# Kernel tuning notes

Measured on AMD Instinct MI355X. Metric: run time of the kernel, lower is better.

## Reference

```python
import jax, jax.numpy as jnp
import numpy as np

MARGIN = 0.3


def _l2norm(x, axis=-1):
    return x / (jnp.linalg.norm(x, axis=axis, keepdims=True) + 1e-12)


def setup_inputs() -> dict:
    key = jax.random.key(0)
    k1, k2, k3, k4 = jax.random.split(key, 4)
    n, P, d = 1024, 8, 2048
    global_feat = jax.random.normal(k1, (n, d), dtype=jnp.float32)
    partial_feat = jax.random.normal(k2, (n, P, d), dtype=jnp.float32)
    part_labels = jax.random.randint(k3, (n, P), 0, 2).astype(jnp.float32)
    global_labels = jax.random.randint(k4, (n,), 0, 64).astype(jnp.int64)
    return {"global_feat": global_feat, "partial_feat": partial_feat,
            "part_labels": part_labels, "global_labels": global_labels}


def reference(global_feat, partial_feat, part_labels, global_labels):
    # --- compute_distance (VGTripletLoss) ---
    g = _l2norm(global_feat)            # [n, d]
    p = _l2norm(partial_feat)           # [n, P, d]
    gs = (1.0 - g @ g.T) / 2.0          # [n, n]
    overlap = part_labels[:, None, :] * part_labels[None, :, :]   # [n, n, P]
    # per-part cosine distance: [n, n, P]
    slf = (1.0 - jnp.einsum('ipd,jpd->ijp', p, p)) / 2.0
    slf = slf * overlap
    dist = (slf.sum(-1) + gs) / (overlap.sum(-1) + 1.0)            # [n, n]

    # --- compute_loss: hard positive/negative mining ---
    mask = global_labels[:, None] == global_labels[None, :]        # [n, n]
    neg_inf = jnp.float32(-1e30)
    pos_inf = jnp.float32(1e30)
    dist_ap = jnp.max(jnp.where(mask, dist, neg_inf), axis=1)      # hardest positive
    dist_an = jnp.min(jnp.where(mask, pos_inf, dist), axis=1)      # hardest negative
    # MarginRankingLoss(y=1, reduction='mean'): max(0, dist_ap - dist_an + margin)
    loss = jnp.mean(jax.nn.relu(dist_ap - dist_an + MARGIN))
    return loss
```

## Files before the change

kernel.cpp:

```cpp
#include <hip/hip_runtime.h>

#define N 1024
#define D 2048
#define P 8
#define F 9
#define KTOT (F * D)
#define BM 128
#define BKT 32
#define MARGIN 0.3f

typedef float f32x4 __attribute__((ext_vector_type(4)));
typedef short s16x8 __attribute__((ext_vector_type(8)));

#define GLOBAL_AS __attribute__((address_space(1)))
#define LDS_AS __attribute__((address_space(3)))

__device__ __forceinline__ const float* feat_row(const float* __restrict__ g,
                                                 const float* __restrict__ p,
                                                 int i, int f) {
    return (f == 0) ? (g + (size_t)i * D)
                    : (p + ((size_t)i * P + (f - 1)) * D);
}

__device__ __forceinline__ unsigned f2bf(float x) {
    unsigned u = __float_as_uint(x);
    return (u + 0x7fffu + ((u >> 16) & 1u)) >> 16;
}

__global__ __launch_bounds__(256)
void pack_kernel(const float* __restrict__ gfeat,
                 const float* __restrict__ pfeat,
                 const float* __restrict__ plab,
                 unsigned short* __restrict__ V) {
    const int wid = (blockIdx.x << 2) | (threadIdx.x >> 6);
    const int lane = threadIdx.x & 63;
    const int i = wid / F, f = wid % F;
    const float* src = feat_row(gfeat, pfeat, i, f);
    const float4* s4 = (const float4*)src;
    float4 a[4][2];
    #pragma unroll
    for (int q = 0; q < 4; ++q) {
        a[q][0] = s4[(q * 64 + lane) * 2];
        a[q][1] = s4[(q * 64 + lane) * 2 + 1];
    }
    float ss = 0.f;
    #pragma unroll
    for (int q = 0; q < 4; ++q)
        #pragma unroll
        for (int h = 0; h < 2; ++h)
            ss += a[q][h].x * a[q][h].x + a[q][h].y * a[q][h].y
                + a[q][h].z * a[q][h].z + a[q][h].w * a[q][h].w;
    #pragma unroll
    for (int m = 32; m > 0; m >>= 1) ss += __shfl_xor(ss, m, 64);
    const float ls = (f == 0) ? 1.0f : plab[i * P + (f - 1)];
    const float inv = ls / (sqrtf(ss) + 1e-12f);
    unsigned short* dst = V + (size_t)wid * D;
    #pragma unroll
    for (int q = 0; q < 4; ++q) {
        uint4 o;
        o.x = f2bf(a[q][0].x * inv) | (f2bf(a[q][0].y * inv) << 16);
        o.y = f2bf(a[q][0].z * inv) | (f2bf(a[q][0].w * inv) << 16);
        o.z = f2bf(a[q][1].x * inv) | (f2bf(a[q][1].y * inv) << 16);
        o.w = f2bf(a[q][1].z * inv) | (f2bf(a[q][1].w * inv) << 16);
        *(uint4*)&dst[(size_t)(q * 64 + lane) * 8] = o;
    }
}

__global__ __launch_bounds__(256)
void gemm_kernel(const unsigned short* __restrict__ V,
                 float* __restrict__ part, int ks) {
    __shared__ short As[BM * BKT];
    __shared__ short Bs[BM * BKT];

    const int nwg = gridDim.x * gridDim.y;
    const int l = blockIdx.x + gridDim.x * blockIdx.y;
    const int q = nwg >> 3;
    const int wg = (l & 7) * q + (l >> 3);
    const int t36 = wg % 36;
    const int bz = wg / 36;

    int by = 0, rem = t36;
    while (rem >= 8 - by) { rem -= 8 - by; ++by; }
    const int bx = by + rem;

    const int t = threadIdx.x;
    const int wave = t >> 6, lane = t & 63;
    const int i0 = by * BM;
    const int j0 = bx * BM;
    const int kbase = bz * ks;
    const int nsteps = ks >> 5;

    const unsigned short* Ap = V + (size_t)(i0 + (t >> 2)) * KTOT + kbase + (t & 3) * 8;
    const unsigned short* Bp = V + (size_t)(j0 + (t >> 2)) * KTOT + kbase + (t & 3) * 8;

    const int kq = lane >> 4;
    const short* Abase = As + ((wave & 1) * 64 + (lane & 15)) * BKT + kq * 8;
    const short* Bbase = Bs + ((wave >> 1) * 64 + (lane & 15)) * BKT + kq * 8;

    f32x4 acc[4][4];
    #pragma unroll
    for (int m = 0; m < 4; ++m)
        #pragma unroll
        for (int n = 0; n < 4; ++n)
            acc[m][n] = (f32x4){0.f, 0.f, 0.f, 0.f};

    for (int ksi = 0; ksi < nsteps; ++ksi) {
        __syncthreads();
        __builtin_amdgcn_global_load_lds((const GLOBAL_AS void*)Ap,
                                         (LDS_AS void*)(As + t * 8), 16, 0, 0);
        __builtin_amdgcn_global_load_lds((const GLOBAL_AS void*)(Ap + (size_t)64 * KTOT),
                                         (LDS_AS void*)(As + 2048 + t * 8), 16, 0, 0);
        __builtin_amdgcn_global_load_lds((const GLOBAL_AS void*)Bp,
                                         (LDS_AS void*)(Bs + t * 8), 16, 0, 0);
        __builtin_amdgcn_global_load_lds((const GLOBAL_AS void*)(Bp + (size_t)64 * KTOT),
                                         (LDS_AS void*)(Bs + 2048 + t * 8), 16, 0, 0);
        Ap += BKT;
        Bp += BKT;
        __syncthreads();

        s16x8 af[4], bf[4];
        #pragma unroll
        for (int m = 0; m < 4; ++m) af[m] = *(const s16x8*)(Abase + m * 16 * BKT);
        #pragma unroll
        for (int n = 0; n < 4; ++n) bf[n] = *(const s16x8*)(Bbase + n * 16 * BKT);
        #pragma unroll
        for (int m = 0; m < 4; ++m)
            #pragma unroll
            for (int n = 0; n < 4; ++n)
                acc[m][n] = __builtin_amdgcn_mfma_f32_16x16x32_bf16(
                    af[m], bf[n], acc[m][n], 0, 0, 0);
    }

    float* outp = part + (size_t)bz * N * N;
    const int rbase = i0 + (wave & 1) * 64 + (lane >> 4) * 4;
    const int cbase = j0 + (wave >> 1) * 64 + (lane & 15);
    #pragma unroll
    for (int m = 0; m < 4; ++m)
        #pragma unroll
        for (int n = 0; n < 4; ++n)
            #pragma unroll
            for (int r = 0; r < 4; ++r)
                outp[(size_t)(rbase + m * 16 + r) * N + cbase + n * 16] = acc[m][n][r];

    if (bx != by) {
        #pragma unroll
        for (int m = 0; m < 4; ++m)
            #pragma unroll
            for (int n = 0; n < 4; ++n)
                #pragma unroll
                for (int r = 0; r < 4; ++r)
                    outp[(size_t)(cbase + n * 16) * N + rbase + m * 16 + r] = acc[m][n][r];
    }
}

template <int S>
__global__ __launch_bounds__(256)
void mine_kernel(const float* __restrict__ part,
                 const float* __restrict__ plab,
                 const int* __restrict__ glab,
                 float* __restrict__ rowloss) {
    const int i = blockIdx.x;
    const int t = threadIdx.x;
    const int wave = t >> 6, lane = t & 63;
    const int j = t * 4;

    float4 dot = {0.f, 0.f, 0.f, 0.f};
    #pragma unroll
    for (int s = 0; s < S; ++s) {
        float4 v = *(const float4*)&part[(size_t)s * N * N + (size_t)i * N + j];
        dot.x += v.x; dot.y += v.y; dot.z += v.z; dot.w += v.w;
    }

    float labj[4][8];
    const float4* pj = (const float4*)&plab[(size_t)j * P];
    #pragma unroll
    for (int q = 0; q < 8; ++q) ((float4*)labj)[q] = pj[q];
    int4 gj = *(const int4*)&glab[j];

    const int li = glab[i];
    float lab_i[P];
    #pragma unroll
    for (int c = 0; c < P; ++c) lab_i[c] = plab[i * P + c];

    float ap = -1e30f, an = 1e30f;
    const float dv[4] = {dot.x, dot.y, dot.z, dot.w};
    const int gv[4] = {gj.x, gj.y, gj.z, gj.w};
    #pragma unroll
    for (int u = 0; u < 4; ++u) {
        float ov = 0.f;
        #pragma unroll
        for (int c = 0; c < P; ++c) ov += lab_i[c] * labj[u][c];
        float d = 0.5f - dv[u] / (2.0f * (ov + 1.0f));
        if (gv[u] == li) ap = fmaxf(ap, d);
        else             an = fminf(an, d);
    }

    #pragma unroll
    for (int m = 32; m > 0; m >>= 1) {
        ap = fmaxf(ap, __shfl_xor(ap, m, 64));
        an = fminf(an, __shfl_xor(an, m, 64));
    }
    __shared__ float sap[4], san[4];
    if (lane == 0) { sap[wave] = ap; san[wave] = an; }
    __syncthreads();
    if (t == 0) {
        float A = fmaxf(fmaxf(sap[0], sap[1]), fmaxf(sap[2], sap[3]));
        float B = fminf(fminf(san[0], san[1]), fminf(san[2], san[3]));
        rowloss[i] = fmaxf(0.f, A - B + MARGIN);
    }
}

__global__ void reduce_kernel(const float* __restrict__ rowloss,
                              float* __restrict__ out) {
    const int t = threadIdx.x;
    float s = rowloss[t] + rowloss[t + 256] + rowloss[t + 512] + rowloss[t + 768];
    __shared__ float red[256];
    red[t] = s;
    __syncthreads();
    for (int st = 128; st > 0; st >>= 1) {
        if (t < st) red[t] += red[t + st];
        __syncthreads();
    }
    if (t == 0) out[0] = red[0] * (1.0f / N);
}

extern "C" void kernel_launch(void* const* d_in, const int* in_sizes, int n_in,
                              void* d_out, int out_size, void* d_ws, size_t ws_size,
                              hipStream_t stream) {
    const float* gfeat = (const float*)d_in[0];
    const float* pfeat = (const float*)d_in[1];
    const float* plab  = (const float*)d_in[2];
    const int*   glab  = (const int*)d_in[3];
    float* out = (float*)d_out;

    const size_t vbytes = (size_t)N * KTOT * 2;
    const size_t slice  = (size_t)N * N * 4;

    int S = (ws_size != 0 && ws_size >= vbytes + 16 * slice + 4096) ? 16 : 8;
    const int ks = KTOT / S;

    char* ws = (char*)d_ws;
    unsigned short* V = (unsigned short*)ws;
    float* part    = (float*)(ws + vbytes);
    float* rowloss = (float*)(ws + vbytes + (size_t)S * slice);

    pack_kernel<<<N * F / 4, 256, 0, stream>>>(gfeat, pfeat, plab, V);
    gemm_kernel<<<dim3(36, S), 256, 0, stream>>>(V, part, ks);
    if (S == 16)
        mine_kernel<16><<<N, 256, 0, stream>>>(part, plab, glab, rowloss);
    else
        mine_kernel<8><<<N, 256, 0, stream>>>(part, plab, glab, rowloss);
    reduce_kernel<<<1, 256, 0, stream>>>(rowloss, out);
}
```

Baseline: 168.2 us.

## Double-buffer LDS tiles in bf16 GEMM to overlap loads with MFMA

Doubles the A and B shared-memory tiles and restructures the K loop so the async global-to-LDS loads for the next step are issued before the MFMAs on the current buffer. This drops one barrier per iteration and aims to hide global load latency behind matrix math. LDS use per workgroup doubles, which may lower occupancy. The compiler may also insert conservative vmcnt waits before the LDS reads, which would remove the intended overlap.

```diff
diff --git a/kernel.cpp b/kernel.cpp
--- a/kernel.cpp
+++ b/kernel.cpp
@@ -69,8 +69,8 @@
 __global__ __launch_bounds__(256)
 void gemm_kernel(const unsigned short* __restrict__ V,
                  float* __restrict__ part, int ks) {
-    __shared__ short As[BM * BKT];
-    __shared__ short Bs[BM * BKT];
+    __shared__ short As[2][BM * BKT];
+    __shared__ short Bs[2][BM * BKT];
 
     const int nwg = gridDim.x * gridDim.y;
     const int l = blockIdx.x + gridDim.x * blockIdx.y;
@@ -94,8 +94,8 @@
     const unsigned short* Bp = V + (size_t)(j0 + (t >> 2)) * KTOT + kbase + (t & 3) * 8;
 
     const int kq = lane >> 4;
-    const short* Abase = As + ((wave & 1) * 64 + (lane & 15)) * BKT + kq * 8;
-    const short* Bbase = Bs + ((wave >> 1) * 64 + (lane & 15)) * BKT + kq * 8;
+    const int aoff = ((wave & 1) * 64 + (lane & 15)) * BKT + kq * 8;
+    const int boff = ((wave >> 1) * 64 + (lane & 15)) * BKT + kq * 8;
 
     f32x4 acc[4][4];
     #pragma unroll
@@ -104,32 +104,48 @@
         for (int n = 0; n < 4; ++n)
             acc[m][n] = (f32x4){0.f, 0.f, 0.f, 0.f};
 
-    for (int ksi = 0; ksi < nsteps; ++ksi) {
+#define STAGE(b) do {                                                          \
+    __builtin_amdgcn_global_load_lds((const GLOBAL_AS void*)Ap,                \
+        (LDS_AS void*)(&As[(b)][0] + t * 8), 16, 0, 0);                        \
+    __builtin_amdgcn_global_load_lds((const GLOBAL_AS void*)(Ap + (size_t)64 * KTOT), \
+        (LDS_AS void*)(&As[(b)][2048] + t * 8), 16, 0, 0);                     \
+    __builtin_amdgcn_global_load_lds((const GLOBAL_AS void*)Bp,                \
+        (LDS_AS void*)(&Bs[(b)][0] + t * 8), 16, 0, 0);                        \
+    __builtin_amdgcn_global_load_lds((const GLOBAL_AS void*)(Bp + (size_t)64 * KTOT), \
+        (LDS_AS void*)(&Bs[(b)][2048] + t * 8), 16, 0, 0);                     \
+    Ap += BKT; Bp += BKT;                                                      \
+} while (0)
+
+#define COMPUTE(b) do {                                                        \
+    s16x8 af[4], bf[4];                                                        \
+    _Pragma("unroll")                                                          \
+    for (int m = 0; m < 4; ++m)                                                \
+        af[m] = *(const s16x8*)(&As[(b)][aoff + m * 16 * BKT]);                \
+    _Pragma("unroll")                                                          \
+    for (int n = 0; n < 4; ++n)                                                \
+        bf[n] = *(const s16x8*)(&Bs[(b)][boff + n * 16 * BKT]);                \
+    _Pragma("unroll")                                                          \
+    for (int m = 0; m < 4; ++m)                                                \
+        _Pragma("unroll")                                                      \
+        for (int n = 0; n < 4; ++n)                                            \
+            acc[m][n] = __builtin_amdgcn_mfma_f32_16x16x32_bf16(               \
+                af[m], bf[n], acc[m][n], 0, 0, 0);                             \
+} while (0)
+
+    STAGE(0);
+    __syncthreads();
+
+    int cur = 0;
+    for (int ksi = 0; ksi < nsteps - 1; ++ksi) {
+        STAGE(cur ^ 1);
+        COMPUTE(cur);
         __syncthreads();
-        __builtin_amdgcn_global_load_lds((const GLOBAL_AS void*)Ap,
-                                         (LDS_AS void*)(As + t * 8), 16, 0, 0);
-        __builtin_amdgcn_global_load_lds((const GLOBAL_AS void*)(Ap + (size_t)64 * KTOT),
-                                         (LDS_AS void*)(As + 2048 + t * 8), 16, 0, 0);
-        __builtin_amdgcn_global_load_lds((const GLOBAL_AS void*)Bp,
-                                         (LDS_AS void*)(Bs + t * 8), 16, 0, 0);
-        __builtin_amdgcn_global_load_lds((const GLOBAL_AS void*)(Bp + (size_t)64 * KTOT),
-                                         (LDS_AS void*)(Bs + 2048 + t * 8), 16, 0, 0);
-        Ap += BKT;
-        Bp += BKT;
-        __syncthreads();
-
-        s16x8 af[4], bf[4];
-        #pragma unroll
-        for (int m = 0; m < 4; ++m) af[m] = *(const s16x8*)(Abase + m * 16 * BKT);
-        #pragma unroll
-        for (int n = 0; n < 4; ++n) bf[n] = *(const s16x8*)(Bbase + n * 16 * BKT);
-        #pragma unroll
-        for (int m = 0; m < 4; ++m)
-            #pragma unroll
-            for (int n = 0; n < 4; ++n)
-                acc[m][n] = __builtin_amdgcn_mfma_f32_16x16x32_bf16(
-                    af[m], bf[n], acc[m][n], 0, 0, 0);
-    }
+        cur ^= 1;
+    }
+    COMPUTE(cur);
+
+#undef STAGE
+#undef COMPUTE
 
     float* outp = part + (size_t)bz * N * N;
     const int rbase = i0 + (wave & 1) * 64 + (lane >> 4) * 4;
```

Result: faster. 164.4 us (-2.3%).
